# Performance work log

Measured on AMD Instinct MI355X. Metric: run time of the kernel, lower is better.

## Reference

```python
import jax, jax.numpy as jnp
import numpy as np

EPS = 1e-7  # K.epsilon()

def squash(v, axis=-1):
    sn = jnp.sum(jnp.square(v), axis=axis, keepdims=True)
    scale = sn / (1.0 + sn) / jnp.sqrt(sn + EPS)
    return scale * v

def setup_inputs() -> dict:
    key = jax.random.key(0)
    k1, k2, k3 = jax.random.split(key, 3)
    B, In, Din = 32, 2048, 8
    N, Dout, C = 64, 16, 32
    x = jax.random.normal(k1, (B, In, Din), dtype=jnp.float32)
    W = jax.random.normal(k2, (N, C, Dout, Din), dtype=jnp.float32) * 0.1
    B_bias = jax.random.normal(k3, (N, Dout), dtype=jnp.float32) * 0.1
    return {"x": x, "W": W, "B_bias": B_bias}

def reference(x, W, B_bias):
    routings = 3
    N, C, Dout, Din = W.shape
    In = x.shape[1]
    # repeat channel weights to cover all input capsules: [N, In, Dout, Din]
    W2 = jnp.repeat(W, In // C, axis=1)
    # vote vectors: inputs_hat[b,n,i,d] = sum_k x[b,i,k] * W2[n,i,d,k]
    inputs_hat = jnp.einsum('bik,nidk->bnid', x, W2)  # [B, N, In, Dout]
    b = jnp.zeros(inputs_hat.shape[:3], dtype=inputs_hat.dtype)  # [B, N, In]
    outputs = None
    for i in range(routings):
        c = jax.nn.softmax(b, axis=1)  # softmax over num_capsule axis
        s = jnp.einsum('bni,bnid->bnd', c, inputs_hat) + B_bias
        outputs = squash(s)
        if i < routings - 1:
            b = b + jnp.einsum('bnd,bnid->bni', outputs, inputs_hat)
    return outputs
```

## Files before the change

kernel.cpp:

```cpp
#include <hip/hip_runtime.h>
#include <math.h>

constexpr int B_    = 32;
constexpr int In_   = 2048;
constexpr int Din_  = 8;
constexpr int N_    = 64;
constexpr int Dout_ = 16;
constexpr int C_    = 32;
constexpr int ICP   = 64;
constexpr float EPS = 1e-7f;

__global__ __launch_bounds__(256) void caps_v0(
    const float* __restrict__ x, const float* __restrict__ W,
    const float* __restrict__ bias, float* __restrict__ v0)
{
    const int b = blockIdx.x >> 3, j = blockIdx.x & 7;
    const int t = threadIdx.x;

    __shared__ float xbar[C_][Din_];

    {
        const int c = t >> 3, k = t & 7;
        const float* xp = x + (size_t)b * In_ * Din_ + (size_t)c * ICP * Din_ + k;
        float acc = 0.f;
        #pragma unroll 8
        for (int i = 0; i < ICP; ++i) acc += xp[i * Din_];
        xbar[c][k] = acc * (1.f / 64.f);
    }
    __syncthreads();

    {
        const int nl = t >> 5, lane32 = t & 31;
        const int d = lane32 >> 1, h = lane32 & 1;
        const int n = j * 8 + nl;

        float a = 0.f;
        #pragma unroll
        for (int cc = 0; cc < 16; ++cc) {
            const int c2 = cc * 2 + h;
            const float4* wp = (const float4*)(W + (((size_t)n * C_ + c2) * Dout_ + d) * Din_);
            const float4 w0 = wp[0], w1 = wp[1];
            a += w0.x * xbar[c2][0] + w0.y * xbar[c2][1] + w0.z * xbar[c2][2] + w0.w * xbar[c2][3]
               + w1.x * xbar[c2][4] + w1.y * xbar[c2][5] + w1.z * xbar[c2][6] + w1.w * xbar[c2][7];
        }
        a += __shfl_xor(a, 1);
        a += bias[n * Dout_ + d];

        float sn = a * a;
        sn += __shfl_xor(sn, 2);
        sn += __shfl_xor(sn, 4);
        sn += __shfl_xor(sn, 8);
        sn += __shfl_xor(sn, 16);
        const float sc = sn / (1.f + sn) / sqrtf(sn + EPS);
        if (h == 0) v0[(size_t)b * 1024 + n * Dout_ + d] = a * sc;
    }
}

__global__ __launch_bounds__(256) void caps_route(
    const float* __restrict__ x, const float* __restrict__ W,
    const float* __restrict__ v_src, float* __restrict__ s_out)
{
    const int b = blockIdx.x >> 5;
    const int c = blockIdx.x & 31;
    const int t = threadIdx.x;
    const int w = t >> 6, l = t & 63;
    const int n4 = t >> 2, q4 = t & 3;

    __shared__ float Us[N_][8];
    __shared__ float xs[ICP][8];
    __shared__ float lg[ICP][68];
    __shared__ float ps[4][ICP];
    __shared__ float inv_s[ICP];
    __shared__ float ys[4][N_][8];

    {
        const float4 vv = *(const float4*)(v_src + ((size_t)b * 64 + n4) * 16 + q4 * 4);
        const float vd[4] = {vv.x, vv.y, vv.z, vv.w};
        float pU[8] = {0, 0, 0, 0, 0, 0, 0, 0};
        #pragma unroll
        for (int dd = 0; dd < 4; ++dd) {
            const int d = q4 * 4 + dd;
            const float4* wp = (const float4*)(W + (((size_t)n4 * 32 + c) * 16 + d) * 8);
            const float4 w0 = wp[0], w1 = wp[1];
            const float v_ = vd[dd];
            pU[0] += v_ * w0.x; pU[1] += v_ * w0.y; pU[2] += v_ * w0.z; pU[3] += v_ * w0.w;
            pU[4] += v_ * w1.x; pU[5] += v_ * w1.y; pU[6] += v_ * w1.z; pU[7] += v_ * w1.w;
        }
        #pragma unroll
        for (int k = 0; k < 8; ++k) {
            pU[k] += __shfl_xor(pU[k], 1);
            pU[k] += __shfl_xor(pU[k], 2);
        }
        float2 u2; u2.x = pU[2 * q4]; u2.y = pU[2 * q4 + 1];
        *(float2*)&Us[n4][2 * q4] = u2;
    }

    float xr[8];
    {
        const float4* xp = (const float4*)(x + ((size_t)b * In_ + c * ICP + l) * 8);
        const float4 x0 = xp[0], x1 = xp[1];
        xr[0] = x0.x; xr[1] = x0.y; xr[2] = x0.z; xr[3] = x0.w;
        xr[4] = x1.x; xr[5] = x1.y; xr[6] = x1.z; xr[7] = x1.w;
        if (w == 0) { *(float4*)&xs[l][0] = x0; *(float4*)&xs[l][4] = x1; }
    }
    __syncthreads();

    {
        float e[16];
        float ssum = 0.f;
        #pragma unroll
        for (int nn = 0; nn < 16; ++nn) {
            const int n = w * 16 + nn;
            const float4 u0 = *(const float4*)&Us[n][0];
            const float4 u1 = *(const float4*)&Us[n][4];
            const float a = u0.x * xr[0] + u0.y * xr[1] + u0.z * xr[2] + u0.w * xr[3]
                          + u1.x * xr[4] + u1.y * xr[5] + u1.z * xr[6] + u1.w * xr[7];
            const float ee = __expf(a);
            e[nn] = ee; ssum += ee;
        }
        #pragma unroll
        for (int qq = 0; qq < 4; ++qq) {
            float4 o;
            o.x = e[qq * 4 + 0]; o.y = e[qq * 4 + 1]; o.z = e[qq * 4 + 2]; o.w = e[qq * 4 + 3];
            *(float4*)&lg[l][w * 16 + qq * 4] = o;
        }
        ps[w][l] = ssum;
    }
    __syncthreads();

    if (t < 64) inv_s[t] = 1.f / (ps[0][t] + ps[1][t] + ps[2][t] + ps[3][t]);
    __syncthreads();

    {
        const int nq = l >> 2, kq = l & 3;
        float y[8] = {0, 0, 0, 0, 0, 0, 0, 0};
        #pragma unroll
        for (int ii = 0; ii < 16; ++ii) {
            const int i = w * 16 + ii;
            const float4 cw = *(const float4*)&lg[i][nq * 4];
            const float iv = inv_s[i];
            const float2 x2 = *(const float2*)&xs[i][kq * 2];
            const float c0 = cw.x * iv, c1 = cw.y * iv, c2 = cw.z * iv, c3 = cw.w * iv;
            y[0] += c0 * x2.x; y[1] += c0 * x2.y;
            y[2] += c1 * x2.x; y[3] += c1 * x2.y;
            y[4] += c2 * x2.x; y[5] += c2 * x2.y;
            y[6] += c3 * x2.x; y[7] += c3 * x2.y;
        }
        #pragma unroll
        for (int jj = 0; jj < 4; ++jj) {
            float2 o; o.x = y[2 * jj]; o.y = y[2 * jj + 1];
            *(float2*)&ys[w][nq * 4 + jj][kq * 2] = o;
        }
    }
    __syncthreads();

    {
        float yn[8];
        #pragma unroll
        for (int k = 0; k < 8; ++k)
            yn[k] = ys[0][n4][k] + ys[1][n4][k] + ys[2][n4][k] + ys[3][n4][k];
        float4 o;
        float* op = (float*)&o;
        #pragma unroll
        for (int dd = 0; dd < 4; ++dd) {
            const int d = q4 * 4 + dd;
            const float4* wp = (const float4*)(W + (((size_t)n4 * 32 + c) * 16 + d) * 8);
            const float4 w0 = wp[0], w1 = wp[1];
            op[dd] = w0.x * yn[0] + w0.y * yn[1] + w0.z * yn[2] + w0.w * yn[3]
                   + w1.x * yn[4] + w1.y * yn[5] + w1.z * yn[6] + w1.w * yn[7];
        }
        *(float4*)(s_out + (((size_t)b * 32 + c) * 64 + n4) * 16 + q4 * 4) = o;
    }
}

__global__ __launch_bounds__(256) void caps_reduce(
    const float* __restrict__ s_src, const float* __restrict__ bias,
    const float* __restrict__ vadd, float* __restrict__ dst)
{
    const int b = blockIdx.x >> 3, j = blockIdx.x & 7;
    const int t = threadIdx.x;
    const int nl = t >> 5, lane32 = t & 31;
    const int d = lane32 >> 1, h = lane32 & 1;
    const int n = j * 8 + nl;

    float a = 0.f;
    #pragma unroll
    for (int cc = 0; cc < 16; ++cc) {
        const int c2 = cc * 2 + h;
        a += s_src[(((size_t)b * 32 + c2) * 64 + n) * 16 + d];
    }
    a += __shfl_xor(a, 1);
    a += bias[n * Dout_ + d];

    float sn = a * a;
    sn += __shfl_xor(sn, 2);
    sn += __shfl_xor(sn, 4);
    sn += __shfl_xor(sn, 8);
    sn += __shfl_xor(sn, 16);
    const float sc = sn / (1.f + sn) / sqrtf(sn + EPS);
    float val = a * sc;
    if (vadd) val += vadd[(size_t)b * 1024 + n * Dout_ + d];
    if (h == 0) dst[(size_t)b * 1024 + n * Dout_ + d] = val;
}

extern "C" void kernel_launch(void* const* d_in, const int* in_sizes, int n_in,
                              void* d_out, int out_size, void* d_ws, size_t ws_size,
                              hipStream_t stream) {
    const float* x    = (const float*)d_in[0];
    const float* W    = (const float*)d_in[1];
    const float* bias = (const float*)d_in[2];
    float* out = (float*)d_out;

    float* ws   = (float*)d_ws;
    float* s1   = ws;
    float* s2   = s1   + (size_t)B_ * C_ * N_ * Dout_;
    float* v0   = s2   + (size_t)B_ * C_ * N_ * Dout_;
    float* vsum = v0   + (size_t)B_ * N_ * Dout_;

    caps_v0    <<<256,  256, 0, stream>>>(x, W, bias, v0);
    caps_route <<<1024, 256, 0, stream>>>(x, W, v0, s1);
    caps_reduce<<<256,  256, 0, stream>>>(s1, bias, v0, vsum);
    caps_route <<<1024, 256, 0, stream>>>(x, W, vsum, s2);
    caps_reduce<<<256,  256, 0, stream>>>(s2, bias, nullptr, out);
}
```

Before: 90.56 us.

## Fuse reduce+squash into route kernel via last-block atomic counter

Removes the separate caps_reduce launches. Each route block writes its partial s, then increments a per-batch atomic counter, and the last of the 32 blocks for that batch sums the partials, applies bias and squash, and writes the output. This saves two kernel launches and the gaps between them, at the cost of a memset, an atomic and a threadfence per block, plus a serialized tail reduction in one block per batch. The partial buffer is shared between the two routing passes, which is safe because of stream ordering.

```diff
diff --git a/kernel.cpp b/kernel.cpp
--- a/kernel.cpp
+++ b/kernel.cpp
@@ -58,7 +58,9 @@
 
 __global__ __launch_bounds__(256) void caps_route(
     const float* __restrict__ x, const float* __restrict__ W,
-    const float* __restrict__ v_src, float* __restrict__ s_out)
+    const float* __restrict__ bias, const float* __restrict__ v_src,
+    float* __restrict__ sp, const float* __restrict__ vadd,
+    float* __restrict__ dst, int* __restrict__ cnt)
 {
     const int b = blockIdx.x >> 5;
     const int c = blockIdx.x & 31;
@@ -72,6 +74,7 @@
     __shared__ float ps[4][ICP];
     __shared__ float inv_s[ICP];
     __shared__ float ys[4][N_][8];
+    __shared__ int   lastflag;
 
     {
         const float4 vv = *(const float4*)(v_src + ((size_t)b * 64 + n4) * 16 + q4 * 4);
@@ -159,8 +162,7 @@
         #pragma unroll
         for (int k = 0; k < 8; ++k)
             yn[k] = ys[0][n4][k] + ys[1][n4][k] + ys[2][n4][k] + ys[3][n4][k];
-        float4 o;
-        float* op = (float*)&o;
+        float4 o; float* op = (float*)&o;
         #pragma unroll
         for (int dd = 0; dd < 4; ++dd) {
             const int d = q4 * 4 + dd;
@@ -169,38 +171,32 @@
             op[dd] = w0.x * yn[0] + w0.y * yn[1] + w0.z * yn[2] + w0.w * yn[3]
                    + w1.x * yn[4] + w1.y * yn[5] + w1.z * yn[6] + w1.w * yn[7];
         }
-        *(float4*)(s_out + (((size_t)b * 32 + c) * 64 + n4) * 16 + q4 * 4) = o;
-    }
-}
-
-__global__ __launch_bounds__(256) void caps_reduce(
-    const float* __restrict__ s_src, const float* __restrict__ bias,
-    const float* __restrict__ vadd, float* __restrict__ dst)
-{
-    const int b = blockIdx.x >> 3, j = blockIdx.x & 7;
-    const int t = threadIdx.x;
-    const int nl = t >> 5, lane32 = t & 31;
-    const int d = lane32 >> 1, h = lane32 & 1;
-    const int n = j * 8 + nl;
-
-    float a = 0.f;
-    #pragma unroll
-    for (int cc = 0; cc < 16; ++cc) {
-        const int c2 = cc * 2 + h;
-        a += s_src[(((size_t)b * 32 + c2) * 64 + n) * 16 + d];
-    }
-    a += __shfl_xor(a, 1);
-    a += bias[n * Dout_ + d];
-
-    float sn = a * a;
-    sn += __shfl_xor(sn, 2);
-    sn += __shfl_xor(sn, 4);
-    sn += __shfl_xor(sn, 8);
-    sn += __shfl_xor(sn, 16);
-    const float sc = sn / (1.f + sn) / sqrtf(sn + EPS);
-    float val = a * sc;
-    if (vadd) val += vadd[(size_t)b * 1024 + n * Dout_ + d];
-    if (h == 0) dst[(size_t)b * 1024 + n * Dout_ + d] = val;
+        *(float4*)(sp + (((size_t)b * 32 + c) * 64 + n4) * 16 + q4 * 4) = o;
+    }
+
+    __syncthreads();
+    __threadfence();
+    if (t == 0) lastflag = (atomicAdd(cnt + b, 1) == 31);
+    __syncthreads();
+
+    if (lastflag) {
+        __threadfence();
+        float4 a = *(const float4*)(bias + n4 * 16 + q4 * 4);
+        for (int cc = 0; cc < 32; ++cc) {
+            const float4 p = *(const float4*)(sp + (((size_t)b * 32 + cc) * 64 + n4) * 16 + q4 * 4);
+            a.x += p.x; a.y += p.y; a.z += p.z; a.w += p.w;
+        }
+        float sn = a.x * a.x + a.y * a.y + a.z * a.z + a.w * a.w;
+        sn += __shfl_xor(sn, 1);
+        sn += __shfl_xor(sn, 2);
+        const float sc = sn / (1.f + sn) / sqrtf(sn + EPS);
+        float4 o; o.x = a.x * sc; o.y = a.y * sc; o.z = a.z * sc; o.w = a.w * sc;
+        if (vadd) {
+            const float4 vv = *(const float4*)(vadd + (size_t)b * 1024 + n4 * 16 + q4 * 4);
+            o.x += vv.x; o.y += vv.y; o.z += vv.z; o.w += vv.w;
+        }
+        *(float4*)(dst + (size_t)b * 1024 + n4 * 16 + q4 * 4) = o;
+    }
 }
 
 extern "C" void kernel_launch(void* const* d_in, const int* in_sizes, int n_in,
@@ -212,14 +208,13 @@
     float* out = (float*)d_out;
 
     float* ws   = (float*)d_ws;
-    float* s1   = ws;
-    float* s2   = s1   + (size_t)B_ * C_ * N_ * Dout_;
-    float* v0   = s2   + (size_t)B_ * C_ * N_ * Dout_;
+    float* sp   = ws;
+    float* v0   = sp   + (size_t)B_ * C_ * N_ * Dout_;
     float* vsum = v0   + (size_t)B_ * N_ * Dout_;
-
-    caps_v0    <<<256,  256, 0, stream>>>(x, W, bias, v0);
-    caps_route <<<1024, 256, 0, stream>>>(x, W, v0, s1);
-    caps_reduce<<<256,  256, 0, stream>>>(s1, bias, v0, vsum);
-    caps_route <<<1024, 256, 0, stream>>>(x, W, vsum, s2);
-    caps_reduce<<<256,  256, 0, stream>>>(s2, bias, nullptr, out);
+    int*   cnt  = (int*)(vsum + (size_t)B_ * N_ * Dout_);
+
+    hipMemsetAsync(cnt, 0, 64 * sizeof(int), stream);
+    caps_v0   <<<256,  256, 0, stream>>>(x, W, bias, v0);
+    caps_route<<<1024, 256, 0, stream>>>(x, W, bias, v0,   sp, v0,      vsum, cnt);
+    caps_route<<<1024, 256, 0, stream>>>(x, W, bias, vsum, sp, nullptr, out,  cnt + 32);
 }
```

After: 277.9 us. +206.9%, slower.
